# Optimization experiments

Measured on AMD Instinct MI355X. Metric: run time of the kernel, lower is better.

## Reference

```python
import jax, jax.numpy as jnp
import numpy as np

N, D, B, R, EF, K = 500000, 128, 512, 32, 64, 10
INF = 1e30  # sentinel distance for dead/duplicate slots


def setup_inputs() -> dict:
    key = jax.random.key(0)
    k1, k2, k3, k4 = jax.random.split(key, 4)
    return {
        "query": jax.random.normal(k1, (B, D), jnp.float32),
        "storage": jax.random.normal(k2, (N, D), jnp.float32),
        "indices": jax.random.randint(k3, (N, R), 0, N, dtype=jnp.int32),
        "entry": jax.random.randint(k4, (B, EF), 0, N, dtype=jnp.int32),
        "k": K,
        "ef_search": EF,
    }


def _merge(ids, dists, expanded, ef):
    # Dedup by node id (prefer the already-expanded copy so nodes are never
    # re-expanded), then keep the ef best candidates by distance.
    key = ids * 2 + (1 - expanded.astype(ids.dtype))  # expanded copy sorts first
    order = jnp.argsort(key)  # stable sort
    ids, dists, expanded = ids[order], dists[order], expanded[order]
    dup = jnp.concatenate([jnp.zeros((1,), bool), ids[1:] == ids[:-1]])
    dists = jnp.where(dup, INF, dists)       # kill duplicate slots
    expanded = jnp.where(dup, True, expanded)  # dead slots never selected
    order = jnp.argsort(dists)
    return ids[order][:ef], dists[order][:ef], expanded[order][:ef]


def _search_one(q, ep, storage, indices, ef):
    # Beam (priority-list) best-first NSW traversal for a single query,
    # ef steps of expand-best-unexpanded, batched-friendly formulation.
    d0 = jnp.sum((storage[ep] - q) ** 2, axis=-1)  # squared-L2 distances
    state = _merge(ep, d0, jnp.zeros(ep.shape, bool), ef)

    def step(carry, _):
        ids, dists, expanded = carry
        sel = jnp.argmin(jnp.where(expanded, INF, dists))  # best open node
        expanded = expanded.at[sel].set(True)
        nbrs = indices[ids[sel]]                           # [R] neighbor ids
        nd = jnp.sum((storage[nbrs] - q) ** 2, axis=-1)    # [R] distances
        carry = _merge(
            jnp.concatenate([ids, nbrs]),
            jnp.concatenate([dists, nd]),
            jnp.concatenate([expanded, jnp.zeros((R,), bool)]),
            ef,
        )
        return carry, None

    (ids, dists, _), _ = jax.lax.scan(step, state, None, length=ef)
    return ids, dists


def reference(query, storage, indices, entry, k, ef_search):
    ids, dists = jax.vmap(_search_one, in_axes=(0, 0, None, None, None))(
        query, entry, storage, indices, ef_search
    )
    return ids[:, :k], dists[:, :k]
```

## Files before the change

kernel.cpp:

```cpp
#include <hip/hip_runtime.h>
#include <stdint.h>

#define DIM 128
#define RNB 32
#define EFS 64
#define KTOP 10
#define INFD 1e30f

typedef unsigned long long u64;

__device__ __forceinline__ u64 shflx64(u64 v, int m) {
    return (u64)__shfl_xor((long long)v, m, 64);
}
__device__ __forceinline__ u64 shfl64(u64 v, int src) {
    return (u64)__shfl((long long)v, src, 64);
}
__device__ __forceinline__ u64 dsperm64(int dst_byte, u64 v) {
    int lo = __builtin_amdgcn_ds_permute(dst_byte, (int)(unsigned)(v & 0xffffffffu));
    int hi = __builtin_amdgcn_ds_permute(dst_byte, (int)(unsigned)(v >> 32));
    return ((u64)(unsigned)hi << 32) | (unsigned)lo;
}

__device__ __forceinline__ void bitonic128(u64 &e0, u64 &e1, int lane) {
    #pragma unroll
    for (int k = 2; k <= 128; k <<= 1) {
        #pragma unroll
        for (int j = k >> 1; j >= 1; j >>= 1) {
            if (j == 64) {
                u64 lo = e0 < e1 ? e0 : e1;
                u64 hi = e0 < e1 ? e1 : e0;
                e0 = lo; e1 = hi;
            } else {
                u64 o0 = shflx64(e0, j);
                u64 o1 = shflx64(e1, j);
                int i0 = lane, i1 = lane + 64;
                bool keepmin0 = ((i0 & k) == 0) == ((i0 & j) == 0);
                bool keepmin1 = ((i1 & k) == 0) == ((i1 & j) == 0);
                e0 = keepmin0 ? (e0 < o0 ? e0 : o0) : (e0 > o0 ? e0 : o0);
                e1 = keepmin1 ? (e1 < o1 ? e1 : o1) : (e1 > o1 ? e1 : o1);
            }
        }
    }
}

__device__ __forceinline__ void merge_slow(int n, int lane,
                                           int* ids_s, float* dst_s, int* exp_s,
                                           int* ids2, float* dst2, int* exp2) {
    __syncthreads();
    {
        int i1 = lane + 64;
        u64 e0 = ((u64)(uint32_t)(ids_s[lane] * 2 + (exp_s[lane] ? 0 : 1)) << 32) | (uint32_t)lane;
        u64 e1 = ~0ULL;
        if (i1 < n)
            e1 = ((u64)(uint32_t)(ids_s[i1] * 2 + (exp_s[i1] ? 0 : 1)) << 32) | (uint32_t)i1;
        bitonic128(e0, e1, lane);

        int id0 = -1, id1 = -1; float d0 = INFD, d1 = INFD; int x0 = 1, x1 = 1;
        { int p = (int)(e0 & 0xffffffffu); id0 = ids_s[p]; d0 = dst_s[p]; x0 = exp_s[p]; }
        if (e1 != ~0ULL) { int p = (int)(e1 & 0xffffffffu); id1 = ids_s[p]; d1 = dst_s[p]; x1 = exp_s[p]; }

        int prev0 = __shfl_up(id0, 1);
        int top0  = __shfl(id0, 63);
        int prev1 = __shfl_up(id1, 1);
        bool dup0 = (lane > 0) && (id0 == prev0);
        bool dup1 = (i1 < n) && (id1 == ((lane == 0) ? top0 : prev1));
        if (dup0) { d0 = INFD; x0 = 1; }
        if (dup1) { d1 = INFD; x1 = 1; }

        ids2[lane] = id0; dst2[lane] = d0; exp2[lane] = x0;
        ids2[i1]   = id1; dst2[i1]   = d1; exp2[i1]   = x1;

        u64 f0 = ((u64)__float_as_uint(d0) << 32) | (uint32_t)lane;
        u64 f1 = (i1 < n) ? (((u64)__float_as_uint(d1) << 32) | (uint32_t)i1) : ~0ULL;
        bitonic128(f0, f1, lane);

        int pf = (int)(f0 & 0xffffffffu);
        int idf = ids2[pf]; float df = dst2[pf]; int xf = exp2[pf];
        __syncthreads();
        ids_s[lane] = idf; dst_s[lane] = df; exp_s[lane] = xf;
    }
    __syncthreads();
}

extern "C" __global__ __launch_bounds__(64, 1)
void nsw_search(const float* __restrict__ query,
                const float* __restrict__ storage,
                const int* __restrict__ indices,
                const int* __restrict__ entry,
                float* __restrict__ out,
                int B) {
    const int b = blockIdx.x;
    const int lane = threadIdx.x;

    __shared__ __align__(16) float q_s[DIM];
    __shared__ int   ids_s[96];
    __shared__ float dst_s[96];
    __shared__ int   exp_s[96];
    __shared__ int   ids2[128];
    __shared__ float dst2[128];
    __shared__ int   exp2[128];

    q_s[lane]      = query[(size_t)b * DIM + lane];
    q_s[64 + lane] = query[(size_t)b * DIM + 64 + lane];
    ids_s[lane] = entry[(size_t)b * EFS + lane];
    exp_s[lane] = 0;
    __syncthreads();

    #pragma unroll
    for (int p = 0; p < 4; ++p) {
        int g = p * 16 + (lane >> 2), sub = lane & 3;
        int id = ids_s[g];
        const float4* row = (const float4*)(storage + (size_t)id * DIM);
        const float4* q4 = (const float4*)q_s;
        float acc = 0.f;
        #pragma unroll
        for (int c = 0; c < 8; ++c) {
            float4 v = row[sub * 8 + c];
            float4 qv = q4[sub * 8 + c];
            float dx = v.x - qv.x; acc = fmaf(dx, dx, acc);
            dx = v.y - qv.y; acc = fmaf(dx, dx, acc);
            dx = v.z - qv.z; acc = fmaf(dx, dx, acc);
            dx = v.w - qv.w; acc = fmaf(dx, dx, acc);
        }
        acc += __shfl_xor(acc, 1);
        acc += __shfl_xor(acc, 2);
        if (sub == 0) dst_s[g] = acc;
    }

    merge_slow(64, lane, ids_s, dst_s, exp_s, ids2, dst2, exp2);

    int   bid = ids_s[lane];
    float bds = dst_s[lane];
    int   bex = exp_s[lane];

    float4 qv0, qv1, qv2, qv3;
    {
        const float4* q4 = (const float4*)q_s;
        int sub = lane & 7;
        qv0 = q4[sub * 4 + 0]; qv1 = q4[sub * 4 + 1];
        qv2 = q4[sub * 4 + 2]; qv3 = q4[sub * 4 + 3];
    }

    int nidx;
    {
        u64 open = __ballot(bex == 0);
        int sel = open ? (int)(__ffsll((long long)open) - 1) : 0;
        int node = __shfl(bid, sel);
        if (lane == sel) bex = 1;
        nidx = indices[(size_t)node * RNB + (lane & 31)];
    }

    float4 va[4][4];
    #pragma unroll
    for (int p = 0; p < 4; ++p) {
        int g = p * 8 + (lane >> 3);
        int idp = __shfl(nidx, g);
        const float4* row = (const float4*)(storage + (size_t)idp * DIM) + (lane & 7) * 4;
        va[p][0] = row[0]; va[p][1] = row[1]; va[p][2] = row[2]; va[p][3] = row[3];
    }

    for (int step = 0; step < EFS; ++step) {
        float accs[4];
        #pragma unroll
        for (int p = 0; p < 4; ++p) {
            float acc = 0.f;
            float4 v;
            v = va[p][0];
            { float dx = v.x - qv0.x; acc = fmaf(dx, dx, acc);
              dx = v.y - qv0.y; acc = fmaf(dx, dx, acc);
              dx = v.z - qv0.z; acc = fmaf(dx, dx, acc);
              dx = v.w - qv0.w; acc = fmaf(dx, dx, acc); }
            v = va[p][1];
            { float dx = v.x - qv1.x; acc = fmaf(dx, dx, acc);
              dx = v.y - qv1.y; acc = fmaf(dx, dx, acc);
              dx = v.z - qv1.z; acc = fmaf(dx, dx, acc);
              dx = v.w - qv1.w; acc = fmaf(dx, dx, acc); }
            v = va[p][2];
            { float dx = v.x - qv2.x; acc = fmaf(dx, dx, acc);
              dx = v.y - qv2.y; acc = fmaf(dx, dx, acc);
              dx = v.z - qv2.z; acc = fmaf(dx, dx, acc);
              dx = v.w - qv2.w; acc = fmaf(dx, dx, acc); }
            v = va[p][3];
            { float dx = v.x - qv3.x; acc = fmaf(dx, dx, acc);
              dx = v.y - qv3.y; acc = fmaf(dx, dx, acc);
              dx = v.z - qv3.z; acc = fmaf(dx, dx, acc);
              dx = v.w - qv3.w; acc = fmaf(dx, dx, acc); }
            acc += __shfl_xor(acc, 1);
            acc += __shfl_xor(acc, 2);
            acc += __shfl_xor(acc, 4);
            accs[p] = acc;
        }
        int l8 = (lane & 7) << 3;
        float t0 = __shfl(accs[0], l8), t1 = __shfl(accs[1], l8);
        float t2 = __shfl(accs[2], l8), t3 = __shfl(accs[3], l8);
        int ps = (lane >> 3) & 3;
        float ndt = (ps & 2) ? ((ps & 1) ? t3 : t2) : ((ps & 1) ? t1 : t0);
        int nid = nidx;

        bool has_inf = (__ballot(bds >= INFD) != 0ull);

        if (!has_inf) {
            unsigned killmask = 0u;
            #pragma unroll
            for (int j = 0; j < RNB; ++j) {
                int idj = __shfl(nid, j);
                u64 beq = __ballot(bid == idj);
                u64 neq = __ballot(nid == idj);
                u64 kj = beq | (neq & ((1ull << j) - 1ull));
                killmask |= (kj ? 1u : 0u) << j;
            }
            bool kill = (killmask >> (lane & 31)) & 1u;
            float dk = kill ? INFD : ndt;
            u64 nkey = ((u64)__float_as_uint(dk) << 27)
                     | ((u64)(unsigned)(nid * 2 + 1) << 7)
                     | (unsigned)(64 + lane);

            int rank = 0;
            #pragma unroll
            for (int j = 0; j < RNB; ++j) {
                u64 kj = shfl64(nkey, j);
                rank += (kj < nkey) ? 1 : 0;
            }
            u64 e1p = dsperm64((lane < 32) ? ((63 - rank) << 2) : 0, nkey);
            u64 K_newmin = ((__ballot(!kill) & 0xffffffffull) != 0ull)
                         ? shfl64(e1p, 63) : ~0ull;

            u64 bkey = ((u64)__float_as_uint(bds) << 27)
                     | ((u64)(unsigned)(bid * 2 + (bex ? 0 : 1)) << 7)
                     | (unsigned)lane;
            u64 bo = __ballot(bex == 0);
            int selb = bo ? (int)(__ffsll((long long)bo) - 1) : 0;
            u64 K_bopen = bo ? shfl64(bkey, selb) : ~0ull;
            u64 K_minopen = (K_bopen < K_newmin) ? K_bopen : K_newmin;
            u64 bkey63 = shfl64(bkey, 63);
            bool fallback = (K_minopen > bkey63);
            int node = fallback ? __shfl(bid, 0)
                                : (int)(((unsigned)((K_minopen >> 7) & 0xFFFFFull)) >> 1);

            nidx = indices[(size_t)node * RNB + (lane & 31)];

            u64 e0 = bkey;
            u64 e1 = (lane < 32) ? ~0ull : e1p;
            { u64 lo = e0 < e1 ? e0 : e1; e0 = lo; }
            #pragma unroll
            for (int j = 32; j >= 1; j >>= 1) {
                u64 o0 = shflx64(e0, j);
                bool keepmin = (lane & j) == 0;
                e0 = keepmin ? (e0 < o0 ? e0 : o0) : (e0 > o0 ? e0 : o0);
            }

            bds = __uint_as_float((unsigned)(e0 >> 27));
            unsigned key1 = (unsigned)((e0 >> 7) & 0xFFFFFull);
            bid = (int)(key1 >> 1);
            bex = (int)((key1 & 1u) ^ 1u);
            if (!fallback && e0 == K_minopen) bex = 1;
        } else {
            ids_s[lane] = bid; dst_s[lane] = bds; exp_s[lane] = bex;
            if (lane < RNB) { ids_s[64 + lane] = nid; dst_s[64 + lane] = ndt; exp_s[64 + lane] = 0; }
            merge_slow(96, lane, ids_s, dst_s, exp_s, ids2, dst2, exp2);
            bid = ids_s[lane]; bds = dst_s[lane]; bex = exp_s[lane];
            u64 open = __ballot(bex == 0);
            int sel = open ? (int)(__ffsll((long long)open) - 1) : 0;
            int node = __shfl(bid, sel);
            if (lane == sel) bex = 1;
            nidx = indices[(size_t)node * RNB + (lane & 31)];
        }

        if (step + 1 < EFS) {
            #pragma unroll
            for (int p = 0; p < 4; ++p) {
                int g = p * 8 + (lane >> 3);
                int idp = __shfl(nidx, g);
                const float4* row = (const float4*)(storage + (size_t)idp * DIM) + (lane & 7) * 4;
                va[p][0] = row[0]; va[p][1] = row[1]; va[p][2] = row[2]; va[p][3] = row[3];
            }
        }
    }

    if (lane < KTOP) {
        out[(size_t)b * KTOP + lane] = (float)bid;
        out[(size_t)B * KTOP + (size_t)b * KTOP + lane] = bds;
    }
}

extern "C" void kernel_launch(void* const* d_in, const int* in_sizes, int n_in,
                              void* d_out, int out_size, void* d_ws, size_t ws_size,
                              hipStream_t stream) {
    const float* query   = (const float*)d_in[0];
    const float* storage = (const float*)d_in[1];
    const int*   indices = (const int*)d_in[2];
    const int*   entry   = (const int*)d_in[3];
    int B = in_sizes[0] / DIM;
    float* out = (float*)d_out;
    nsw_search<<<B, 64, 0, stream>>>(query, storage, indices, entry, out, B);
}
```

Before: 227.2 us.

## Cache neighbor index rows in LDS and prefetch next adjacency speculatively

Adds a 512-set direct-mapped LDS cache of neighbor-index rows. For each candidate just fetched, the 32 lanes prefetch that neighbor's adjacency row into registers, then store it into the cache. This lets the next expansion's index lookup often hit LDS instead of a dependent global load. The duplicate kill mask and beam-state keys are computed one step early, off the critical path, and several shuffles become readlanes. The initial distance loads are batched into registers. The cost is extra global traffic for rows that may never be used, larger LDS use, and more register pressure.

```diff
diff --git a/kernel.cpp b/kernel.cpp
--- a/kernel.cpp
+++ b/kernel.cpp
@@ -6,6 +6,7 @@
 #define EFS 64
 #define KTOP 10
 #define INFD 1e30f
+#define NSET 512
 
 typedef unsigned long long u64;
 
@@ -19,6 +20,14 @@
     int lo = __builtin_amdgcn_ds_permute(dst_byte, (int)(unsigned)(v & 0xffffffffu));
     int hi = __builtin_amdgcn_ds_permute(dst_byte, (int)(unsigned)(v >> 32));
     return ((u64)(unsigned)hi << 32) | (unsigned)lo;
+}
+__device__ __forceinline__ u64 readlane64(u64 v, int l) {
+    unsigned lo = (unsigned)__builtin_amdgcn_readlane((int)(unsigned)(v & 0xffffffffu), l);
+    unsigned hi = (unsigned)__builtin_amdgcn_readlane((int)(unsigned)(v >> 32), l);
+    return ((u64)hi << 32) | lo;
+}
+__device__ __forceinline__ int hset(int id) {
+    return (id ^ (id >> 9)) & (NSET - 1);
 }
 
 __device__ __forceinline__ void bitonic128(u64 &e0, u64 &e1, int lane) {
@@ -82,6 +91,51 @@
     __syncthreads();
 }
 
+#define PROBE_AND_PREFETCH(NODE) do {                                          \
+    int set_n_ = hset(NODE);                                                   \
+    int tg_ = tag_s[set_n_];                                                   \
+    if (tg_ == (NODE)) nid = row_s[set_n_][lane & 31];                         \
+    else               nid = indices[(size_t)(NODE) * RNB + (lane & 31)];      \
+    _Pragma("unroll")                                                          \
+    for (int p_ = 0; p_ < 4; ++p_) {                                           \
+        int g_ = p_ * 8 + (lane >> 3);                                         \
+        int idp_ = __shfl(nid, g_);                                            \
+        const float4* row_ = (const float4*)(storage + (size_t)idp_ * DIM) + (lane & 7) * 4; \
+        va[p_][0] = row_[0]; va[p_][1] = row_[1];                              \
+        va[p_][2] = row_[2]; va[p_][3] = row_[3];                              \
+    }                                                                          \
+    if (lane < RNB) {                                                          \
+        const int4* ip_ = (const int4*)(indices + (size_t)nid * RNB);          \
+        _Pragma("unroll")                                                      \
+        for (int c_ = 0; c_ < 8; ++c_) ir[c_] = ip_[c_];                       \
+    }                                                                          \
+} while (0)
+
+#define POSTMERGE_STATE() do {                                                 \
+    killmask = 0u;                                                             \
+    _Pragma("unroll")                                                          \
+    for (int j_ = 0; j_ < RNB; ++j_) {                                         \
+        int idj_ = __builtin_amdgcn_readlane(nid, j_);                         \
+        u64 beq_ = __ballot(bid == idj_);                                      \
+        u64 neq_ = __ballot(nid == idj_);                                      \
+        u64 kj_ = beq_ | (neq_ & ((1ull << j_) - 1ull));                       \
+        killmask |= (kj_ ? 1u : 0u) << j_;                                     \
+    }                                                                          \
+    setl = hset(nid);                                                          \
+    lose = false;                                                              \
+    _Pragma("unroll")                                                          \
+    for (int j_ = 0; j_ < RNB; ++j_) {                                         \
+        int sj_ = __builtin_amdgcn_readlane(setl, j_);                         \
+        lose = lose || ((setl == sj_) && ((lane & 31) < j_));                  \
+    }                                                                          \
+    u64 bkeyN_ = ((u64)__float_as_uint(bds) << 27)                             \
+               | ((u64)(unsigned)(bid * 2 + (bex ? 0 : 1)) << 7)               \
+               | (unsigned)lane;                                               \
+    bkey63 = readlane64(bkeyN_, 63);                                           \
+    u64 bo_ = __ballot(bex == 0);                                              \
+    K_bopen = bo_ ? readlane64(bkeyN_, (int)(__ffsll((long long)bo_) - 1)) : ~0ull; \
+} while (0)
+
 extern "C" __global__ __launch_bounds__(64, 1)
 void nsw_search(const float* __restrict__ query,
                 const float* __restrict__ storage,
@@ -93,6 +147,8 @@
     const int lane = threadIdx.x;
 
     __shared__ __align__(16) float q_s[DIM];
+    __shared__ int tag_s[NSET];
+    __shared__ __align__(16) int row_s[NSET][RNB];
     __shared__ int   ids_s[96];
     __shared__ float dst_s[96];
     __shared__ int   exp_s[96];
@@ -100,31 +156,46 @@
     __shared__ float dst2[128];
     __shared__ int   exp2[128];
 
+    #pragma unroll
+    for (int c = 0; c < NSET / 64; ++c) tag_s[c * 64 + lane] = -1;
+
     q_s[lane]      = query[(size_t)b * DIM + lane];
     q_s[64 + lane] = query[(size_t)b * DIM + 64 + lane];
     ids_s[lane] = entry[(size_t)b * EFS + lane];
     exp_s[lane] = 0;
     __syncthreads();
 
-    #pragma unroll
-    for (int p = 0; p < 4; ++p) {
-        int g = p * 16 + (lane >> 2), sub = lane & 3;
-        int id = ids_s[g];
-        const float4* row = (const float4*)(storage + (size_t)id * DIM);
-        const float4* q4 = (const float4*)q_s;
-        float acc = 0.f;
+    {
+        float4 ea[16];
         #pragma unroll
-        for (int c = 0; c < 8; ++c) {
-            float4 v = row[sub * 8 + c];
-            float4 qv = q4[sub * 8 + c];
-            float dx = v.x - qv.x; acc = fmaf(dx, dx, acc);
-            dx = v.y - qv.y; acc = fmaf(dx, dx, acc);
-            dx = v.z - qv.z; acc = fmaf(dx, dx, acc);
-            dx = v.w - qv.w; acc = fmaf(dx, dx, acc);
-        }
-        acc += __shfl_xor(acc, 1);
-        acc += __shfl_xor(acc, 2);
-        if (sub == 0) dst_s[g] = acc;
+        for (int batch = 0; batch < 2; ++batch) {
+            #pragma unroll
+            for (int pp = 0; pp < 2; ++pp) {
+                int p = batch * 2 + pp, g = p * 16 + (lane >> 2), sub = lane & 3;
+                int id = ids_s[g];
+                const float4* row = (const float4*)(storage + (size_t)id * DIM);
+                #pragma unroll
+                for (int c = 0; c < 8; ++c) ea[pp * 8 + c] = row[sub * 8 + c];
+            }
+            #pragma unroll
+            for (int pp = 0; pp < 2; ++pp) {
+                int p = batch * 2 + pp, g = p * 16 + (lane >> 2), sub = lane & 3;
+                const float4* q4 = (const float4*)q_s;
+                float acc = 0.f;
+                #pragma unroll
+                for (int c = 0; c < 8; ++c) {
+                    float4 v = ea[pp * 8 + c];
+                    float4 qv = q4[sub * 8 + c];
+                    float dx = v.x - qv.x; acc = fmaf(dx, dx, acc);
+                    dx = v.y - qv.y; acc = fmaf(dx, dx, acc);
+                    dx = v.z - qv.z; acc = fmaf(dx, dx, acc);
+                    dx = v.w - qv.w; acc = fmaf(dx, dx, acc);
+                }
+                acc += __shfl_xor(acc, 1);
+                acc += __shfl_xor(acc, 2);
+                if (sub == 0) dst_s[g] = acc;
+            }
+        }
     }
 
     merge_slow(64, lane, ids_s, dst_s, exp_s, ids2, dst2, exp2);
@@ -141,25 +212,26 @@
         qv2 = q4[sub * 4 + 2]; qv3 = q4[sub * 4 + 3];
     }
 
-    int nidx;
+    int nid;
+    float4 va[4][4];
+    int4 ir[8];
+    unsigned killmask = 0;
+    int  setl = 0;
+    bool lose = false;
+    u64  K_bopen, bkey63;
+
     {
         u64 open = __ballot(bex == 0);
         int sel = open ? (int)(__ffsll((long long)open) - 1) : 0;
         int node = __shfl(bid, sel);
         if (lane == sel) bex = 1;
-        nidx = indices[(size_t)node * RNB + (lane & 31)];
-    }
-
-    float4 va[4][4];
-    #pragma unroll
-    for (int p = 0; p < 4; ++p) {
-        int g = p * 8 + (lane >> 3);
-        int idp = __shfl(nidx, g);
-        const float4* row = (const float4*)(storage + (size_t)idp * DIM) + (lane & 7) * 4;
-        va[p][0] = row[0]; va[p][1] = row[1]; va[p][2] = row[2]; va[p][3] = row[3];
+        PROBE_AND_PREFETCH(node);
+        POSTMERGE_STATE();
     }
 
     for (int step = 0; step < EFS; ++step) {
+        const bool lastit = (step + 1 == EFS);
+
         float accs[4];
         #pragma unroll
         for (int p = 0; p < 4; ++p) {
@@ -195,50 +267,42 @@
         float t2 = __shfl(accs[2], l8), t3 = __shfl(accs[3], l8);
         int ps = (lane >> 3) & 3;
         float ndt = (ps & 2) ? ((ps & 1) ? t3 : t2) : ((ps & 1) ? t1 : t0);
-        int nid = nidx;
+
+        if (lane < RNB && !lose) {
+            tag_s[setl] = nid;
+            #pragma unroll
+            for (int c = 0; c < 8; ++c) *(int4*)&row_s[setl][c * 4] = ir[c];
+        }
 
         bool has_inf = (__ballot(bds >= INFD) != 0ull);
 
         if (!has_inf) {
-            unsigned killmask = 0u;
-            #pragma unroll
-            for (int j = 0; j < RNB; ++j) {
-                int idj = __shfl(nid, j);
-                u64 beq = __ballot(bid == idj);
-                u64 neq = __ballot(nid == idj);
-                u64 kj = beq | (neq & ((1ull << j) - 1ull));
-                killmask |= (kj ? 1u : 0u) << j;
-            }
             bool kill = (killmask >> (lane & 31)) & 1u;
             float dk = kill ? INFD : ndt;
             u64 nkey = ((u64)__float_as_uint(dk) << 27)
                      | ((u64)(unsigned)(nid * 2 + 1) << 7)
-                     | (unsigned)(64 + lane);
+                     | (unsigned)(64 + (lane & 31));
 
             int rank = 0;
             #pragma unroll
             for (int j = 0; j < RNB; ++j) {
-                u64 kj = shfl64(nkey, j);
+                u64 kj = readlane64(nkey, j);
                 rank += (kj < nkey) ? 1 : 0;
             }
-            u64 e1p = dsperm64((lane < 32) ? ((63 - rank) << 2) : 0, nkey);
-            u64 K_newmin = ((__ballot(!kill) & 0xffffffffull) != 0ull)
-                         ? shfl64(e1p, 63) : ~0ull;
+            u64 rz = __ballot(rank == 0) & 0xffffffffull;
+            u64 K_newmin = readlane64(nkey, (int)(__ffsll((long long)rz) - 1));
+            u64 K_minopen = (K_bopen < K_newmin) ? K_bopen : K_newmin;
+            bool fallback = (K_minopen > bkey63);
+            int node = fallback ? __builtin_amdgcn_readlane(bid, 0)
+                                : (int)(((unsigned)((K_minopen >> 7) & 0xFFFFFu)) >> 1);
 
             u64 bkey = ((u64)__float_as_uint(bds) << 27)
                      | ((u64)(unsigned)(bid * 2 + (bex ? 0 : 1)) << 7)
                      | (unsigned)lane;
-            u64 bo = __ballot(bex == 0);
-            int selb = bo ? (int)(__ffsll((long long)bo) - 1) : 0;
-            u64 K_bopen = bo ? shfl64(bkey, selb) : ~0ull;
-            u64 K_minopen = (K_bopen < K_newmin) ? K_bopen : K_newmin;
-            u64 bkey63 = shfl64(bkey, 63);
-            bool fallback = (K_minopen > bkey63);
-            int node = fallback ? __shfl(bid, 0)
-                                : (int)(((unsigned)((K_minopen >> 7) & 0xFFFFFull)) >> 1);
-
-            nidx = indices[(size_t)node * RNB + (lane & 31)];
-
+
+            if (!lastit) PROBE_AND_PREFETCH(node);
+
+            u64 e1p = dsperm64((lane < 32) ? ((63 - rank) << 2) : 0, nkey);
             u64 e0 = bkey;
             u64 e1 = (lane < 32) ? ~0ull : e1p;
             { u64 lo = e0 < e1 ? e0 : e1; e0 = lo; }
@@ -248,9 +312,8 @@
                 bool keepmin = (lane & j) == 0;
                 e0 = keepmin ? (e0 < o0 ? e0 : o0) : (e0 > o0 ? e0 : o0);
             }
-
             bds = __uint_as_float((unsigned)(e0 >> 27));
-            unsigned key1 = (unsigned)((e0 >> 7) & 0xFFFFFull);
+            unsigned key1 = (unsigned)((e0 >> 7) & 0xFFFFFu);
             bid = (int)(key1 >> 1);
             bex = (int)((key1 & 1u) ^ 1u);
             if (!fallback && e0 == K_minopen) bex = 1;
@@ -263,18 +326,10 @@
             int sel = open ? (int)(__ffsll((long long)open) - 1) : 0;
             int node = __shfl(bid, sel);
             if (lane == sel) bex = 1;
-            nidx = indices[(size_t)node * RNB + (lane & 31)];
-        }
-
-        if (step + 1 < EFS) {
-            #pragma unroll
-            for (int p = 0; p < 4; ++p) {
-                int g = p * 8 + (lane >> 3);
-                int idp = __shfl(nidx, g);
-                const float4* row = (const float4*)(storage + (size_t)idp * DIM) + (lane & 7) * 4;
-                va[p][0] = row[0]; va[p][1] = row[1]; va[p][2] = row[2]; va[p][3] = row[3];
-            }
-        }
+            if (!lastit) PROBE_AND_PREFETCH(node);
+        }
+
+        if (!lastit) POSTMERGE_STATE();
     }
 
     if (lane < KTOP) {
```

Measured after the change: 395.8 us. 74.2% more time.
